# Kernel tuning notes

Measured on AMD Instinct MI355X. Metric: run time of the kernel, lower is better.

## Reference

```python
import jax, jax.numpy as jnp
import numpy as np

N_NODES = 100000
N_EDGES = 1600000
IN_FEAT = 64
OUT_FEAT = 64
NUM_RELS = 8
NUM_BASES = 4


def setup_inputs() -> dict:
    key = jax.random.key(0)
    ks = jax.random.split(key, 9)
    feat = jax.random.normal(ks[0], (N_NODES, IN_FEAT), dtype=jnp.float32)
    src = jax.random.randint(ks[1], (N_EDGES,), 0, N_NODES, dtype=jnp.int64)
    dst = jax.random.randint(ks[2], (N_EDGES,), 0, N_NODES, dtype=jnp.int64)
    etypes = jax.random.randint(ks[3], (N_EDGES,), 0, NUM_RELS, dtype=jnp.int64)
    norm = jax.random.uniform(ks[4], (N_EDGES, 1), dtype=jnp.float32)
    # learned parameters (xavier-uniform-like scaling)
    def xavier(k, shape):
        fan_in, fan_out = shape[-2], shape[-1]
        lim = jnp.sqrt(6.0 / (fan_in + fan_out)).astype(jnp.float32)
        return jax.random.uniform(k, shape, jnp.float32, -lim, lim)
    weight = xavier(ks[5], (NUM_BASES, IN_FEAT, OUT_FEAT))
    w_comp = xavier(ks[6], (NUM_RELS, NUM_BASES))
    h_bias = jnp.zeros((OUT_FEAT,), dtype=jnp.float32)
    loop_weight = xavier(ks[7], (IN_FEAT, OUT_FEAT))
    return {"feat": feat, "src": src, "dst": dst, "etypes": etypes,
            "norm": norm, "weight": weight, "w_comp": w_comp,
            "h_bias": h_bias, "loop_weight": loop_weight}


def reference(feat, src, dst, etypes, norm, weight, w_comp, h_bias, loop_weight):
    # Basis decomposition: W_r = sum_b w_comp[r,b] * V_b.
    # Per-edge message m_e = feat[src_e] @ W_{etype_e} * norm_e, computed as:
    #   proj[n,b,:] = feat[n] @ V_b   (project nodes once per basis)
    #   m_e = sum_b w_comp[etype_e, b] * proj[src_e, b, :]
    # which is mathematically identical and avoids an [E, in, out] weight gather.
    proj = jnp.einsum('ni,bio->nbo', feat, weight)      # [N, B, out]
    coef = w_comp[etypes]                               # [E, B]
    msg = jnp.einsum('eb,ebo->eo', coef, proj[src])     # [E, out]
    msg = msg * norm                                    # edge normalizer
    # Aggregate (sum) into destination nodes
    agg = jax.ops.segment_sum(msg, dst, num_segments=feat.shape[0])  # [N, out]
    # bias + self-loop message
    out = agg + h_bias + feat @ loop_weight
    return out
```

## Files before the change

### kernel.cpp

```cpp
#include <hip/hip_runtime.h>
#include <hip/hip_bf16.h>


constexpr int NNODES = 100000;
constexpr int NEDGES = 1600000;

constexpr size_t WF_BYTES  = (size_t)NNODES * 512 * 2;
constexpr size_t HEADE_OFF = WF_BYTES;
constexpr size_t REC_OFF   = HEADE_OFF + (size_t)NNODES * 4;
constexpr size_t WS_NEED_E = REC_OFF + (size_t)NEDGES * 16;
constexpr size_t HEAD_OFF  = WF_BYTES;
constexpr size_t NEXT_OFF  = HEAD_OFF + (size_t)NNODES * 4;
constexpr size_t WS_NEED   = NEXT_OFF + (size_t)NEDGES * 4;

template <int PATH>
__global__ __launch_bounds__(256)
void rgcn_proj(const float* __restrict__ feat,
               const float* __restrict__ weight,
               const float* __restrict__ w_comp,
               const float* __restrict__ h_bias,
               const float* __restrict__ loop_w,
               __hip_bfloat16* __restrict__ table,
               float* __restrict__ out)
{
    __shared__ float featl[32 * 64];

    const int t = threadIdx.x;
    const int nbase = blockIdx.x * 32;

    {
        const float4* fsrc = (const float4*)(feat + (size_t)nbase * 64);
        float4* fdst = (float4*)featl;
        fdst[t] = fsrc[t];
        fdst[t + 256] = fsrc[t + 256];
    }

    const int lane = t & 63;
    const int n0 = (t >> 6) * 8;
    const float bias = h_bias[lane];

    __syncthreads();

    constexpr int NM = (PATH == 2) ? 1 : 5;
    float acc[8][NM];
    #pragma unroll
    for (int n = 0; n < 8; ++n)
        #pragma unroll
        for (int m = 0; m < NM; ++m)
            acc[n][m] = 0.0f;

    #pragma unroll 4
    for (int i0 = 0; i0 < 64; i0 += 4) {
        float4 f4[8];
        #pragma unroll
        for (int n = 0; n < 8; ++n)
            f4[n] = *(const float4*)&featl[(n0 + n) * 64 + i0];
        #pragma unroll
        for (int q = 0; q < 4; ++q) {
            const int i = i0 + q;
            float vv[NM];
            if (PATH < 2) {
                #pragma unroll
                for (int b = 0; b < 4; ++b)
                    vv[b] = weight[b * 4096 + i * 64 + lane];
                vv[4] = loop_w[i * 64 + lane];
            } else {
                vv[0] = loop_w[i * 64 + lane];
            }
            #pragma unroll
            for (int n = 0; n < 8; ++n) {
                const float fv = (q == 0) ? f4[n].x : (q == 1) ? f4[n].y
                               : (q == 2) ? f4[n].z : f4[n].w;
                #pragma unroll
                for (int m = 0; m < NM; ++m)
                    acc[n][m] = fmaf(fv, vv[m], acc[n][m]);
            }
        }
    }

    float wc[8][4];
    if (PATH == 0) {
        #pragma unroll
        for (int r = 0; r < 8; ++r)
            #pragma unroll
            for (int b = 0; b < 4; ++b)
                wc[r][b] = w_comp[r * 4 + b];
    }

    #pragma unroll
    for (int n = 0; n < 8; ++n) {
        const size_t gn = (size_t)(nbase + n0 + n);
        out[gn * 64 + lane] = bias + acc[n][NM - 1];
        if (PATH == 0) {
            #pragma unroll
            for (int r = 0; r < 8; ++r) {
                const float w = fmaf(wc[r][0], acc[n][0],
                                fmaf(wc[r][1], acc[n][1],
                                fmaf(wc[r][2], acc[n][2],
                                     wc[r][3] * acc[n][3])));
                table[gn * 512 + (size_t)r * 64 + lane] = __float2bfloat16(w);
            }
        } else if (PATH == 1) {
            #pragma unroll
            for (int b = 0; b < 4; ++b)
                table[gn * 256 + (size_t)b * 64 + lane] = __float2bfloat16(acc[n][b]);
        }
    }
}

__global__ __launch_bounds__(256)
void k_link_emb(const int* __restrict__ src, const int* __restrict__ dst,
                const int* __restrict__ et, const float* __restrict__ norm,
                int* __restrict__ head, int4* __restrict__ rec)
{
    const int i = blockIdx.x * blockDim.x + threadIdx.x;
    const int stride = gridDim.x * blockDim.x;
    for (int e = i; e < NEDGES; e += stride) {
        const int d = dst[e];
        const int s = src[e];
        const int r = et[e];
        const float nm = norm[e];
        const int old = atomicExch(&head[d], e);
        rec[e] = make_int4(old, s * 512 + r * 64, __float_as_int(nm), 0);
    }
}

__global__ __launch_bounds__(256)
void k_agg_emb(const int* __restrict__ head, const int4* __restrict__ rec,
               const __hip_bfloat16* __restrict__ wfeat,
               float* __restrict__ out)
{
    const int lane = threadIdx.x & 63;
    const int wid = (int)((blockIdx.x * blockDim.x + threadIdx.x) >> 6);
    const int n0 = wid * 8;

    int   e[8];
    float acc[8];
    bool alive = false;
    #pragma unroll
    for (int k = 0; k < 8; ++k) {
        e[k] = head[n0 + k];
        acc[k] = 0.0f;
        alive = alive || (e[k] >= 0);
    }

    while (alive) {
        int4 R[8];
        #pragma unroll
        for (int k = 0; k < 8; ++k) {
            const int idx = (e[k] >= 0) ? e[k] : 0;
            R[k] = rec[idx];
        }
        float w[8];
        #pragma unroll
        for (int k = 0; k < 8; ++k)
            w[k] = __bfloat162float(wfeat[(size_t)R[k].y + lane]);
        alive = false;
        #pragma unroll
        for (int k = 0; k < 8; ++k) {
            if (e[k] >= 0) {
                acc[k] = fmaf(__int_as_float(R[k].z), w[k], acc[k]);
                e[k] = R[k].x;
            }
            alive = alive || (e[k] >= 0);
        }
    }

    #pragma unroll
    for (int k = 0; k < 8; ++k)
        out[(size_t)(n0 + k) * 64 + lane] += acc[k];
}

__global__ __launch_bounds__(256)
void k_link(const int* __restrict__ dst, int* __restrict__ head,
            int* __restrict__ next)
{
    const int i = blockIdx.x * blockDim.x + threadIdx.x;
    const int stride = gridDim.x * blockDim.x;
    for (int e = i; e < NEDGES; e += stride) {
        const int d = dst[e];
        const int old = atomicExch(&head[d], e);
        next[e] = old;
    }
}

__global__ __launch_bounds__(256)
void k_agg(const int* __restrict__ head, const int* __restrict__ next,
           const int* __restrict__ src, const int* __restrict__ et,
           const float* __restrict__ norm,
           const __hip_bfloat16* __restrict__ wfeat,
           float* __restrict__ out)
{
    const int lane = threadIdx.x & 63;
    const int wid = (int)((blockIdx.x * blockDim.x + threadIdx.x) >> 6);
    const int n0 = wid * 8;

    int   e[8];
    float acc[8];
    #pragma unroll
    for (int k = 0; k < 8; ++k) {
        e[k] = head[n0 + k];
        acc[k] = 0.0f;
    }

    while (true) {
        bool progress = false;
        #pragma unroll
        for (int k = 0; k < 8; ++k) {
            const int ek = e[k];
            if (ek >= 0) {
                progress = true;
                const int   s = src[ek];
                const int   r = et[ek];
                const float m = norm[ek];
                const float w = __bfloat162float(
                    wfeat[(size_t)s * 512 + (size_t)r * 64 + lane]);
                acc[k] = fmaf(m, w, acc[k]);
                e[k] = next[ek];
            }
        }
        if (!progress) break;
    }

    #pragma unroll
    for (int k = 0; k < 8; ++k)
        out[(size_t)(n0 + k) * 64 + lane] += acc[k];
}

__global__ __launch_bounds__(256)
void rgcn_edge_a(const int* __restrict__ src, const int* __restrict__ dst,
                 const int* __restrict__ et, const float* __restrict__ norm,
                 const __hip_bfloat16* __restrict__ wfeat,
                 float* __restrict__ out)
{
    const int lane = threadIdx.x & 63;
    const int wid  = (int)((blockIdx.x * blockDim.x + threadIdx.x) >> 6);
    const int nw   = (int)((gridDim.x * blockDim.x) >> 6);
    for (int e = wid; e < NEDGES; e += nw) {
        const int   s  = src[e];
        const int   d  = dst[e];
        const int   r  = et[e];
        const float nm = norm[e];
        const float w  = __bfloat162float(wfeat[(size_t)s * 512 + (size_t)r * 64 + lane]);
        atomicAdd(out + (size_t)d * 64 + lane, w * nm);
    }
}

__global__ __launch_bounds__(256)
void rgcn_edge_b(const int* __restrict__ src, const int* __restrict__ dst,
                 const int* __restrict__ et, const float* __restrict__ norm,
                 const __hip_bfloat16* __restrict__ proj,
                 const float* __restrict__ w_comp,
                 float* __restrict__ out)
{
    const int lane = threadIdx.x & 63;
    const int wid  = (int)((blockIdx.x * blockDim.x + threadIdx.x) >> 6);
    const int nw   = (int)((gridDim.x * blockDim.x) >> 6);
    for (int e = wid; e < NEDGES; e += nw) {
        const int   s  = src[e];
        const int   d  = dst[e];
        const int   r  = et[e];
        const float nm = norm[e];
        const __hip_bfloat16* p = proj + (size_t)s * 256;
        float m = w_comp[r * 4 + 0] * __bfloat162float(p[lane]);
        m = fmaf(w_comp[r * 4 + 1], __bfloat162float(p[ 64 + lane]), m);
        m = fmaf(w_comp[r * 4 + 2], __bfloat162float(p[128 + lane]), m);
        m = fmaf(w_comp[r * 4 + 3], __bfloat162float(p[192 + lane]), m);
        atomicAdd(out + (size_t)d * 64 + lane, m * nm);
    }
}

__global__ __launch_bounds__(256)
void rgcn_edge_c(const int* __restrict__ src, const int* __restrict__ dst,
                 const int* __restrict__ et, const float* __restrict__ norm,
                 const float* __restrict__ feat,
                 const float* __restrict__ weight,
                 const float* __restrict__ w_comp,
                 float* __restrict__ out)
{
    __shared__ __hip_bfloat16 Vl[4 * 64 * 64];
    const int t = threadIdx.x;
    #pragma unroll
    for (int k = 0; k < 64; ++k)
        Vl[t + k * 256] = __float2bfloat16(weight[t + k * 256]);
    __syncthreads();

    const int lane = t & 63;
    const int wid  = (int)((blockIdx.x * blockDim.x + t) >> 6);
    const int nw   = (int)((gridDim.x * blockDim.x) >> 6);
    for (int e = wid; e < NEDGES; e += nw) {
        const int   s  = src[e];
        const int   d  = dst[e];
        const int   r  = et[e];
        const float nm = norm[e];
        const float wc0 = w_comp[r * 4 + 0], wc1 = w_comp[r * 4 + 1];
        const float wc2 = w_comp[r * 4 + 2], wc3 = w_comp[r * 4 + 3];
        const float f = feat[(size_t)s * 64 + lane];
        float acc = 0.0f;
        #pragma unroll 8
        for (int i = 0; i < 64; ++i) {
            const float fi = __shfl(f, i);
            float w =        wc0 * __bfloat162float(Vl[          i * 64 + lane]);
            w = fmaf(wc1, __bfloat162float(Vl[ 4096 + i * 64 + lane]), w);
            w = fmaf(wc2, __bfloat162float(Vl[ 8192 + i * 64 + lane]), w);
            w = fmaf(wc3, __bfloat162float(Vl[12288 + i * 64 + lane]), w);
            acc = fmaf(fi, w, acc);
        }
        atomicAdd(out + (size_t)d * 64 + lane, acc * nm);
    }
}

extern "C" void kernel_launch(void* const* d_in, const int* in_sizes, int n_in,
                              void* d_out, int out_size, void* d_ws, size_t ws_size,
                              hipStream_t stream) {
    const float* feat   = (const float*)d_in[0];
    const int*   src    = (const int*)  d_in[1];
    const int*   dst    = (const int*)  d_in[2];
    const int*   et     = (const int*)  d_in[3];
    const float* norm   = (const float*)d_in[4];
    const float* weight = (const float*)d_in[5];
    const float* w_comp = (const float*)d_in[6];
    const float* h_bias = (const float*)d_in[7];
    const float* loop_w = (const float*)d_in[8];
    float* out = (float*)d_out;
    char* ws = (char*)d_ws;

    const dim3 gridP(NNODES / 32);

    if (ws_size >= WS_NEED_E) {
        __hip_bfloat16* wfeat = (__hip_bfloat16*)ws;
        int*  head = (int*)(ws + HEADE_OFF);
        int4* rec  = (int4*)(ws + REC_OFF);

        hipMemsetAsync(head, 0xFF, (size_t)NNODES * 4, stream);
        hipLaunchKernelGGL(k_link_emb, dim3(2048), dim3(256), 0, stream,
                           src, dst, et, norm, head, rec);
        hipLaunchKernelGGL((rgcn_proj<0>), gridP, dim3(256), 0, stream,
                           feat, weight, w_comp, h_bias, loop_w, wfeat, out);
        hipLaunchKernelGGL(k_agg_emb, dim3(NNODES / 32), dim3(256), 0, stream,
                           head, rec, wfeat, out);
    } else if (ws_size >= WS_NEED) {
        __hip_bfloat16* wfeat = (__hip_bfloat16*)ws;
        int* head = (int*)(ws + HEAD_OFF);
        int* next = (int*)(ws + NEXT_OFF);

        hipMemsetAsync(head, 0xFF, (size_t)NNODES * 4, stream);
        hipLaunchKernelGGL(k_link, dim3(2048), dim3(256), 0, stream,
                           dst, head, next);
        hipLaunchKernelGGL((rgcn_proj<0>), gridP, dim3(256), 0, stream,
                           feat, weight, w_comp, h_bias, loop_w, wfeat, out);
        hipLaunchKernelGGL(k_agg, dim3(NNODES / 32), dim3(256), 0, stream,
                           head, next, src, et, norm, wfeat, out);
    } else if (ws_size >= WF_BYTES) {
        __hip_bfloat16* wfeat = (__hip_bfloat16*)ws;
        hipLaunchKernelGGL((rgcn_proj<0>), gridP, dim3(256), 0, stream,
                           feat, weight, w_comp, h_bias, loop_w, wfeat, out);
        hipLaunchKernelGGL(rgcn_edge_a, dim3(2048), dim3(256), 0, stream,
                           src, dst, et, norm, wfeat, out);
    } else if (ws_size >= (size_t)NNODES * 256 * 2) {
        __hip_bfloat16* proj = (__hip_bfloat16*)ws;
        hipLaunchKernelGGL((rgcn_proj<1>), gridP, dim3(256), 0, stream,
                           feat, weight, w_comp, h_bias, loop_w, proj, out);
        hipLaunchKernelGGL(rgcn_edge_b, dim3(2048), dim3(256), 0, stream,
                           src, dst, et, norm, proj, w_comp, out);
    } else {
        hipLaunchKernelGGL((rgcn_proj<2>), gridP, dim3(256), 0, stream,
                           feat, weight, w_comp, h_bias, loop_w,
                           (__hip_bfloat16*)nullptr, out);
        hipLaunchKernelGGL(rgcn_edge_c, dim3(2048), dim3(256), 0, stream,
                           src, dst, et, norm, feat, weight, w_comp, out);
    }
}
```

Before: 348.1 us.

## Compute per-relation node projections with bf16 MFMA using a precombined weight matrix

Adds a small kernel that folds the basis weights and w_comp into per-relation weights, concatenates the self-loop weight, and stores the result as one bf16 [576x64] matrix. A new projection kernel stages 32 nodes of features in LDS as bf16 and uses MFMA 16x16x32 bf16 instructions to produce all 8 relation projections plus the self-loop output. Results go through LDS for coalesced wide stores. This replaces scalar FMA projection work with matrix cores, at the cost of bf16 rounding of the features and the self-loop product, plus an extra kernel launch and a larger workspace requirement.

```diff
diff --git a/kernel.cpp b/kernel.cpp
--- a/kernel.cpp
+++ b/kernel.cpp
@@ -9,9 +9,189 @@
 constexpr size_t HEADE_OFF = WF_BYTES;
 constexpr size_t REC_OFF   = HEADE_OFF + (size_t)NNODES * 4;
 constexpr size_t WS_NEED_E = REC_OFF + (size_t)NEDGES * 16;
+constexpr size_t WCAT_OFF  = WS_NEED_E;
+constexpr size_t WS_NEED_M = WCAT_OFF + (size_t)576 * 64 * 2;
 constexpr size_t HEAD_OFF  = WF_BYTES;
 constexpr size_t NEXT_OFF  = HEAD_OFF + (size_t)NNODES * 4;
 constexpr size_t WS_NEED   = NEXT_OFF + (size_t)NEDGES * 4;
+
+typedef __attribute__((ext_vector_type(8))) short short8v;
+typedef __attribute__((ext_vector_type(4))) float f32x4;
+
+__global__ __launch_bounds__(256)
+void k_wcat(const float* __restrict__ weight, const float* __restrict__ w_comp,
+            const float* __restrict__ loop_w, __hip_bfloat16* __restrict__ wcat)
+{
+    const int idx = blockIdx.x * 256 + threadIdx.x;
+    if (idx >= 576 * 64) return;
+    const int c = idx >> 6, i = idx & 63;
+    float v;
+    if (c < 512) {
+        const int r = c >> 6, o = c & 63;
+        v = w_comp[r * 4 + 0] * weight[        i * 64 + o]
+          + w_comp[r * 4 + 1] * weight[ 4096 + i * 64 + o]
+          + w_comp[r * 4 + 2] * weight[ 8192 + i * 64 + o]
+          + w_comp[r * 4 + 3] * weight[12288 + i * 64 + o];
+    } else {
+        v = loop_w[i * 64 + (c - 512)];
+    }
+    wcat[(size_t)c * 64 + i] = __float2bfloat16(v);
+}
+
+__global__ __launch_bounds__(256)
+void proj_mfma(const float* __restrict__ feat,
+               const __hip_bfloat16* __restrict__ wcat,
+               const float* __restrict__ h_bias,
+               __hip_bfloat16* __restrict__ wfeat,
+               float* __restrict__ out)
+{
+    __shared__ __hip_bfloat16 Alds[32 * 72];
+    __shared__ __hip_bfloat16 Clds[32 * 520];
+
+    const int t = threadIdx.x;
+    const int lane = t & 63;
+    const int wv = t >> 6;
+    const int nbase = blockIdx.x * 32;
+
+    {
+        const float4* fsrc = (const float4*)(feat + (size_t)nbase * 64);
+        #pragma unroll
+        for (int kk = 0; kk < 2; ++kk) {
+            const int idx = t + kk * 256;
+            const float4 f = fsrc[idx];
+            const int row = idx >> 4;
+            const int c4  = (idx & 15) * 4;
+            __hip_bfloat16* p = &Alds[row * 72 + c4];
+            p[0] = __float2bfloat16(f.x);
+            p[1] = __float2bfloat16(f.y);
+            p[2] = __float2bfloat16(f.z);
+            p[3] = __float2bfloat16(f.w);
+        }
+    }
+    __syncthreads();
+
+    const int colbase = wv * 144;
+    const int lr = lane & 15;
+    const int lg = lane >> 4;
+
+    f32x4 acc[2][9];
+    #pragma unroll
+    for (int mf = 0; mf < 2; ++mf)
+        #pragma unroll
+        for (int nf = 0; nf < 9; ++nf)
+            acc[mf][nf] = (f32x4){0.f, 0.f, 0.f, 0.f};
+
+    #pragma unroll
+    for (int ks = 0; ks < 2; ++ks) {
+        short8v a[2];
+        #pragma unroll
+        for (int mf = 0; mf < 2; ++mf)
+            a[mf] = *(const short8v*)&Alds[(mf * 16 + lr) * 72 + ks * 32 + lg * 8];
+        short8v b[9];
+        #pragma unroll
+        for (int nf = 0; nf < 9; ++nf) {
+            const int col = colbase + nf * 16 + lr;
+            b[nf] = *(const short8v*)&wcat[(size_t)col * 64 + ks * 32 + lg * 8];
+        }
+        #pragma unroll
+        for (int mf = 0; mf < 2; ++mf)
+            #pragma unroll
+            for (int nf = 0; nf < 9; ++nf)
+                acc[mf][nf] = __builtin_amdgcn_mfma_f32_16x16x32_bf16(
+                    a[mf], b[nf], acc[mf][nf], 0, 0, 0);
+    }
+
+    #pragma unroll
+    for (int mf = 0; mf < 2; ++mf) {
+        #pragma unroll
+        for (int nf = 0; nf < 9; ++nf) {
+            const int gc = colbase + nf * 16 + lr;
+            const int mrow = mf * 16 + lg * 4;
+            if (gc < 512) {
+                #pragma unroll
+                for (int q = 0; q < 4; ++q)
+                    Clds[(mrow + q) * 520 + gc] = __float2bfloat16(acc[mf][nf][q]);
+            } else {
+                const int o = gc - 512;
+                const float bias = h_bias[o];
+                #pragma unroll
+                for (int q = 0; q < 4; ++q)
+                    out[(size_t)(nbase + mrow + q) * 64 + o] = bias + acc[mf][nf][q];
+            }
+        }
+    }
+    __syncthreads();
+
+    #pragma unroll
+    for (int p = 0; p < 8; ++p) {
+        const int node = p * 4 + wv;
+        const uint4 v = *(const uint4*)&Clds[node * 520 + lane * 8];
+        *(uint4*)((char*)(wfeat + (size_t)(nbase + node) * 512) + lane * 16) = v;
+    }
+}
+
+__global__ __launch_bounds__(256)
+void k_link_emb(const int* __restrict__ src, const int* __restrict__ dst,
+                const int* __restrict__ et, const float* __restrict__ norm,
+                int* __restrict__ head, int4* __restrict__ rec)
+{
+    const int i = blockIdx.x * blockDim.x + threadIdx.x;
+    const int stride = gridDim.x * blockDim.x;
+    for (int e = i; e < NEDGES; e += stride) {
+        const int d = dst[e];
+        const int s = src[e];
+        const int r = et[e];
+        const float nm = norm[e];
+        const int old = atomicExch(&head[d], e);
+        rec[e] = make_int4(old, s * 512 + r * 64, __float_as_int(nm), 0);
+    }
+}
+
+__global__ __launch_bounds__(256)
+void k_agg_emb(const int* __restrict__ head, const int4* __restrict__ rec,
+               const __hip_bfloat16* __restrict__ wfeat,
+               float* __restrict__ out)
+{
+    const int lane = threadIdx.x & 63;
+    const int wid = (int)((blockIdx.x * blockDim.x + threadIdx.x) >> 6);
+    const int n0 = wid * 8;
+
+    int   e[8];
+    float acc[8];
+    bool alive = false;
+    #pragma unroll
+    for (int k = 0; k < 8; ++k) {
+        e[k] = head[n0 + k];
+        acc[k] = 0.0f;
+        alive = alive || (e[k] >= 0);
+    }
+
+    while (alive) {
+        int4 R[8];
+        #pragma unroll
+        for (int k = 0; k < 8; ++k) {
+            const int idx = (e[k] >= 0) ? e[k] : 0;
+            R[k] = rec[idx];
+        }
+        float w[8];
+        #pragma unroll
+        for (int k = 0; k < 8; ++k)
+            w[k] = __bfloat162float(wfeat[(size_t)R[k].y + lane]);
+        alive = false;
+        #pragma unroll
+        for (int k = 0; k < 8; ++k) {
+            if (e[k] >= 0) {
+                acc[k] = fmaf(__int_as_float(R[k].z), w[k], acc[k]);
+                e[k] = R[k].x;
+            }
+            alive = alive || (e[k] >= 0);
+        }
+    }
+
+    #pragma unroll
+    for (int k = 0; k < 8; ++k)
+        out[(size_t)(n0 + k) * 64 + lane] += acc[k];
+}
 
 template <int PATH>
 __global__ __launch_bounds__(256)
@@ -106,69 +286,6 @@
                 table[gn * 256 + (size_t)b * 64 + lane] = __float2bfloat16(acc[n][b]);
         }
     }
-}
-
-__global__ __launch_bounds__(256)
-void k_link_emb(const int* __restrict__ src, const int* __restrict__ dst,
-                const int* __restrict__ et, const float* __restrict__ norm,
-                int* __restrict__ head, int4* __restrict__ rec)
-{
-    const int i = blockIdx.x * blockDim.x + threadIdx.x;
-    const int stride = gridDim.x * blockDim.x;
-    for (int e = i; e < NEDGES; e += stride) {
-        const int d = dst[e];
-        const int s = src[e];
-        const int r = et[e];
-        const float nm = norm[e];
-        const int old = atomicExch(&head[d], e);
-        rec[e] = make_int4(old, s * 512 + r * 64, __float_as_int(nm), 0);
-    }
-}
-
-__global__ __launch_bounds__(256)
-void k_agg_emb(const int* __restrict__ head, const int4* __restrict__ rec,
-               const __hip_bfloat16* __restrict__ wfeat,
-               float* __restrict__ out)
-{
-    const int lane = threadIdx.x & 63;
-    const int wid = (int)((blockIdx.x * blockDim.x + threadIdx.x) >> 6);
-    const int n0 = wid * 8;
-
-    int   e[8];
-    float acc[8];
-    bool alive = false;
-    #pragma unroll
-    for (int k = 0; k < 8; ++k) {
-        e[k] = head[n0 + k];
-        acc[k] = 0.0f;
-        alive = alive || (e[k] >= 0);
-    }
-
-    while (alive) {
-        int4 R[8];
-        #pragma unroll
-        for (int k = 0; k < 8; ++k) {
-            const int idx = (e[k] >= 0) ? e[k] : 0;
-            R[k] = rec[idx];
-        }
-        float w[8];
-        #pragma unroll
-        for (int k = 0; k < 8; ++k)
-            w[k] = __bfloat162float(wfeat[(size_t)R[k].y + lane]);
-        alive = false;
-        #pragma unroll
-        for (int k = 0; k < 8; ++k) {
-            if (e[k] >= 0) {
-                acc[k] = fmaf(__int_as_float(R[k].z), w[k], acc[k]);
-                e[k] = R[k].x;
-            }
-            alive = alive || (e[k] >= 0);
-        }
-    }
-
-    #pragma unroll
-    for (int k = 0; k < 8; ++k)
-        out[(size_t)(n0 + k) * 64 + lane] += acc[k];
 }
 
 __global__ __launch_bounds__(256)
@@ -327,7 +444,22 @@
 
     const dim3 gridP(NNODES / 32);
 
-    if (ws_size >= WS_NEED_E) {
+    if (ws_size >= WS_NEED_M) {
+        __hip_bfloat16* wfeat = (__hip_bfloat16*)ws;
+        int*  head = (int*)(ws + HEADE_OFF);
+        int4* rec  = (int4*)(ws + REC_OFF);
+        __hip_bfloat16* wcat = (__hip_bfloat16*)(ws + WCAT_OFF);
+
+        hipMemsetAsync(head, 0xFF, (size_t)NNODES * 4, stream);
+        hipLaunchKernelGGL(k_wcat, dim3(144), dim3(256), 0, stream,
+                           weight, w_comp, loop_w, wcat);
+        hipLaunchKernelGGL(k_link_emb, dim3(2048), dim3(256), 0, stream,
+                           src, dst, et, norm, head, rec);
+        hipLaunchKernelGGL(proj_mfma, gridP, dim3(256), 0, stream,
+                           feat, wcat, h_bias, wfeat, out);
+        hipLaunchKernelGGL(k_agg_emb, dim3(NNODES / 32), dim3(256), 0, stream,
+                           head, rec, wfeat, out);
+    } else if (ws_size >= WS_NEED_E) {
         __hip_bfloat16* wfeat = (__hip_bfloat16*)ws;
         int*  head = (int*)(ws + HEADE_OFF);
         int4* rec  = (int4*)(ws + REC_OFF);
```

After: 316.8 us. -9.0%, faster.
